# Kernel optimization log

Hardware: AMD Instinct MI355X
Metric: run time of the kernel (lower is better)

## Reference

```python
import jax, jax.numpy as jnp
import numpy as np

B, S, A, C = 32, 52, 3, 80  # batch, grid, anchors-per-cell, classes
EPS_LOG = 1e-16
EPS_IOU = 1e-6
L_CLASS, L_NOOBJ, L_OBJ, L_BOX = 1.0, 10.0, 1.0, 10.0


def setup_inputs() -> dict:
    key = jax.random.key(0)
    k_obj, k_xy, k_wh, k_cls, k_pred, k_anc = jax.random.split(key, 6)
    # target (B,S,S,3,6): [obj_flag, x, y, w, h, class_id]
    obj = (jax.random.uniform(k_obj, (B, S, S, A)) < 0.05).astype(jnp.float32)
    xy = jax.random.uniform(k_xy, (B, S, S, A, 2))
    wh = jax.random.uniform(k_wh, (B, S, S, A, 2), minval=0.1, maxval=2.0)
    cls = jax.random.randint(k_cls, (B, S, S, A), 0, C).astype(jnp.float32)
    target = jnp.concatenate([obj[..., None], xy, wh, cls[..., None]], axis=-1)
    pred = jax.random.normal(k_pred, (B, S, S, A * (C + 5)), dtype=jnp.float32)
    anchors = jax.random.uniform(k_anc, (A, 2), minval=0.5, maxval=2.0)
    return {"target": target, "pred": pred, "anchors": anchors}


def _iou_midpoint(b1, b2):
    # boxes [..., 4] = (cx, cy, w, h)
    b1x1, b1y1 = b1[..., 0] - b1[..., 2] / 2, b1[..., 1] - b1[..., 3] / 2
    b1x2, b1y2 = b1[..., 0] + b1[..., 2] / 2, b1[..., 1] + b1[..., 3] / 2
    b2x1, b2y1 = b2[..., 0] - b2[..., 2] / 2, b2[..., 1] - b2[..., 3] / 2
    b2x2, b2y2 = b2[..., 0] + b2[..., 2] / 2, b2[..., 1] + b2[..., 3] / 2
    iw = jnp.clip(jnp.minimum(b1x2, b2x2) - jnp.maximum(b1x1, b2x1), 0.0)
    ih = jnp.clip(jnp.minimum(b1y2, b2y2) - jnp.maximum(b1y1, b2y1), 0.0)
    inter = iw * ih
    a1 = jnp.abs((b1x2 - b1x1) * (b1y2 - b1y1))
    a2 = jnp.abs((b2x2 - b2x1) * (b2y2 - b2y1))
    return inter / (a1 + a2 - inter + EPS_IOU)


def reference(target, pred, anchors):
    b, s1, s2, k = pred.shape
    prediction = pred.reshape(b, s1, s2, A, k // A)  # (B,S,S,3,C+5)
    obj_f = (target[..., 0] == 1.0).astype(pred.dtype)     # (B,S,S,3)
    noobj_f = (target[..., 0] == 0.0).astype(pred.dtype)
    n_obj = jnp.maximum(jnp.sum(obj_f), 1.0)
    n_noobj = jnp.maximum(jnp.sum(noobj_f), 1.0)

    # ---- no-object BCE (from logits), mean over masked elems ----
    logit_o = prediction[..., 0]
    y = target[..., 0]
    bce = jnp.maximum(logit_o, 0.0) - logit_o * y + jnp.log1p(jnp.exp(-jnp.abs(logit_o)))
    noobjloss = jnp.sum(bce * noobj_f) / n_noobj

    # ---- class sparse CE (from logits), mean over obj cells ----
    logp = jax.nn.log_softmax(prediction[..., 5:], axis=-1)
    labels = target[..., 5].astype(jnp.int32)
    ce = -jnp.take_along_axis(logp, labels[..., None], axis=-1)[..., 0]
    classloss = jnp.sum(ce * obj_f) / n_obj

    # ---- box MSE in transformed space ----
    anc = anchors.reshape(1, 1, 1, A, 2)
    pred_xy = jax.nn.sigmoid(prediction[..., 1:3])
    tgt_wh_log = jnp.log(EPS_LOG + target[..., 3:5] / anc)
    tgt_box = jnp.concatenate([target[..., 1:3], tgt_wh_log], axis=-1)   # (B,S,S,3,4)
    pred_box_reg = jnp.concatenate([pred_xy, prediction[..., 3:5]], axis=-1)
    sq = (tgt_box - pred_box_reg) ** 2
    boxloss = jnp.sum(sq * obj_f[..., None]) / (4.0 * n_obj)

    # ---- objectness MSE against IoU (note: original code compares decoded
    # pred box to the LOG-transformed target wh, faithfully reproduced) ----
    box_pred = jnp.concatenate([pred_xy, jnp.exp(prediction[..., 3:5]) * anc], axis=-1)
    iou = _iou_midpoint(box_pred, tgt_box)                  # (B,S,S,3)
    objloss = jnp.sum(((iou * target[..., 0] - logit_o) ** 2) * obj_f) / n_obj

    return (L_NOOBJ * noobjloss + L_CLASS * classloss
            + L_BOX * boxloss + L_OBJ * objloss)
```

## Files before the change

kernel.cpp:

```cpp
#include <hip/hip_runtime.h>
#include <math.h>

#define BB 32
#define SS 52
#define AA 3
#define CC 80

constexpr int N_CELL = BB * SS * SS;
constexpr int N_ANCH = N_CELL * AA;
constexpr int BLOCK  = 256;
constexpr int NBLK   = N_ANCH / BLOCK;

__device__ __forceinline__ float fast_rcp(float x) {
    return __builtin_amdgcn_rcpf(x);
}


__global__ __launch_bounds__(BLOCK) void yolo_main(
    const float* __restrict__ target,
    const float* __restrict__ pred,
    const float* __restrict__ anchors,
    float* __restrict__ ws)
{
    const int tid  = threadIdx.x;
    const int n    = blockIdx.x * BLOCK + tid;
    const int lane = tid & 63;
    const int grp  = lane >> 4;
    const int l16  = lane & 15;

    const int cell = n / 3;
    const int a    = n - cell * 3;
    const float* t = target + (size_t)n * 6;
    const int poff = cell * 255 + a * 85;

    const float2 t01 = *reinterpret_cast<const float2*>(t);
    const float  l   = pred[poff];
    const bool isobj = (t01.x != 0.0f);

    float2 t23, t45;
    float p1, p2, p3, p4, aw, ah;
    if (isobj) {
        t23 = *reinterpret_cast<const float2*>(t + 2);
        t45 = *reinterpret_cast<const float2*>(t + 4);
        p1 = pred[poff + 1];
        p2 = pred[poff + 2];
        p3 = pred[poff + 3];
        p4 = pred[poff + 4];
        aw = anchors[a * 2 + 0];
        ah = anchors[a * 2 + 1];
    }

    float s_obj = 0.f, s_noobj = 0.f, s_bce = 0.f, s_ce = 0.f, s_sq = 0.f, s_objt = 0.f;
    int label_l = 0;

    if (!isobj) {
        s_noobj = 1.0f;
        s_bce   = fmaxf(l, 0.0f) + __logf(1.0f + __expf(-fabsf(l)));
    } else {
        s_obj   = 1.0f;
        label_l = (int)t45.y;

        float px = fast_rcp(1.0f + __expf(-p1));
        float py = fast_rcp(1.0f + __expf(-p2));
        float tx = t01.y, ty = t23.x;
        float tw = __logf(1e-16f + t23.y * fast_rcp(aw));
        float th = __logf(1e-16f + t45.x * fast_rcp(ah));
        float dx = tx - px, dy = ty - py, dw = tw - p3, dh = th - p4;
        s_sq = dx * dx + dy * dy + dw * dw + dh * dh;

        float bw = __expf(p3) * aw;
        float bh = __expf(p4) * ah;
        float b1x1 = px - bw * 0.5f, b1x2 = px + bw * 0.5f;
        float b1y1 = py - bh * 0.5f, b1y2 = py + bh * 0.5f;
        float b2x1 = tx - tw * 0.5f, b2x2 = tx + tw * 0.5f;
        float b2y1 = ty - th * 0.5f, b2y2 = ty + th * 0.5f;
        float iw = fmaxf(fminf(b1x2, b2x2) - fmaxf(b1x1, b2x1), 0.0f);
        float ih = fmaxf(fminf(b1y2, b2y2) - fmaxf(b1y1, b2y1), 0.0f);
        float inter = iw * ih;
        float a1 = fabsf((b1x2 - b1x1) * (b1y2 - b1y1));
        float a2 = fabsf((b2x2 - b2x1) * (b2y2 - b2y1));
        float iou = inter * fast_rcp(a1 + a2 - inter + 1e-6f);
        float d = iou - l;
        s_objt = d * d;
    }

    unsigned long long m = __ballot(isobj);
    while (m) {
        int b0 = -1, b1 = -1, b2 = -1, b3 = -1;
        if (m) { b0 = __ffsll(m) - 1; m &= m - 1; }
        if (m) { b1 = __ffsll(m) - 1; m &= m - 1; }
        if (m) { b2 = __ffsll(m) - 1; m &= m - 1; }
        if (m) { b3 = __ffsll(m) - 1; m &= m - 1; }
        int src = (grp == 0) ? b0 : (grp == 1) ? b1 : (grp == 2) ? b2 : b3;
        bool active = (src >= 0);
        int s = active ? src : 0;
        int offu  = __shfl(poff, s, 64) + 5;
        int label = __shfl(label_l, s, 64);
        const float* cl = pred + offu + l16 * 5;

        float v0 = 0.f, v1 = 0.f, v2 = 0.f, v3 = 0.f, v4 = 0.f;
        if (active) { v0 = cl[0]; v1 = cl[1]; v2 = cl[2]; v3 = cl[3]; v4 = cl[4]; }

        float mx = fmaxf(fmaxf(fmaxf(v0, v1), fmaxf(v2, v3)), v4);
        #pragma unroll
        for (int o = 8; o > 0; o >>= 1) mx = fmaxf(mx, __shfl_xor(mx, o, 16));

        float se = __expf(v0 - mx) + __expf(v1 - mx) + __expf(v2 - mx)
                 + __expf(v3 - mx) + __expf(v4 - mx);
        #pragma unroll
        for (int o = 8; o > 0; o >>= 1) se += __shfl_xor(se, o, 16);

        int e = label % 5;
        float cand = (e == 0) ? v0 : (e == 1) ? v1 : (e == 2) ? v2
                   : (e == 3) ? v3 : v4;
        float cll  = __shfl(cand, (grp << 4) + label / 5, 64);

        if (active && l16 == 0) s_ce += (mx + __logf(se)) - cll;
    }

    #pragma unroll
    for (int off = 32; off > 0; off >>= 1) {
        s_obj   += __shfl_down(s_obj,   off, 64);
        s_noobj += __shfl_down(s_noobj, off, 64);
        s_bce   += __shfl_down(s_bce,   off, 64);
        s_ce    += __shfl_down(s_ce,    off, 64);
        s_sq    += __shfl_down(s_sq,    off, 64);
        s_objt  += __shfl_down(s_objt,  off, 64);
    }

    __shared__ float red[4][6];
    int wave = tid >> 6;
    if ((tid & 63) == 0) {
        red[wave][0] = s_obj;  red[wave][1] = s_noobj; red[wave][2] = s_bce;
        red[wave][3] = s_ce;   red[wave][4] = s_sq;    red[wave][5] = s_objt;
    }
    __syncthreads();
    if (tid < 6) {
        float v = red[0][tid] + red[1][tid] + red[2][tid] + red[3][tid];
        ws[(size_t)blockIdx.x * 6 + tid] = v;
    }
}

__global__ __launch_bounds__(256) void yolo_final(const float* __restrict__ ws,
                                                  float* __restrict__ out) {
    float acc[6] = {0.f, 0.f, 0.f, 0.f, 0.f, 0.f};
    for (int b = threadIdx.x; b < NBLK; b += 256) {
        const float* p = ws + (size_t)b * 6;
        float2 p01 = *reinterpret_cast<const float2*>(p);
        float2 p23 = *reinterpret_cast<const float2*>(p + 2);
        float2 p45 = *reinterpret_cast<const float2*>(p + 4);
        acc[0] += p01.x; acc[1] += p01.y; acc[2] += p23.x;
        acc[3] += p23.y; acc[4] += p45.x; acc[5] += p45.y;
    }
    #pragma unroll
    for (int off = 32; off > 0; off >>= 1) {
        #pragma unroll
        for (int k = 0; k < 6; ++k) acc[k] += __shfl_down(acc[k], off, 64);
    }
    __shared__ float red[4][6];
    int wave = threadIdx.x >> 6;
    if ((threadIdx.x & 63) == 0) {
        #pragma unroll
        for (int k = 0; k < 6; ++k) red[wave][k] = acc[k];
    }
    __syncthreads();
    if (threadIdx.x == 0) {
        float t[6];
        #pragma unroll
        for (int k = 0; k < 6; ++k)
            t[k] = red[0][k] + red[1][k] + red[2][k] + red[3][k];
        float n_obj   = fmaxf(t[0], 1.0f);
        float n_noobj = fmaxf(t[1], 1.0f);
        float noobjloss = t[2] / n_noobj;
        float classloss = t[3] / n_obj;
        float boxloss   = t[4] / (4.0f * n_obj);
        float objloss   = t[5] / n_obj;
        out[0] = 10.0f * noobjloss + 1.0f * classloss + 10.0f * boxloss + 1.0f * objloss;
    }
}

extern "C" void kernel_launch(void* const* d_in, const int* in_sizes, int n_in,
                              void* d_out, int out_size, void* d_ws, size_t ws_size,
                              hipStream_t stream) {
    const float* target  = (const float*)d_in[0];
    const float* pred    = (const float*)d_in[1];
    const float* anchors = (const float*)d_in[2];
    float* out = (float*)d_out;
    float* ws  = (float*)d_ws;

    hipLaunchKernelGGL(yolo_main, dim3(NBLK), dim3(BLOCK), 0, stream,
                       target, pred, anchors, ws);

    hipLaunchKernelGGL(yolo_final, dim3(1), dim3(256), 0, stream, ws, out);
}
```

Before: 17.43 us.

## Hoist loads and prefetch first class-logit batch before per-anchor math

```diff
diff --git a/kernel.cpp b/kernel.cpp
--- a/kernel.cpp
+++ b/kernel.cpp
@@ -10,6 +10,7 @@
 constexpr int N_ANCH = N_CELL * AA;
 constexpr int BLOCK  = 256;
 constexpr int NBLK   = N_ANCH / BLOCK;
+constexpr int WSCOL  = 1024;
 
 __device__ __forceinline__ float fast_rcp(float x) {
     return __builtin_amdgcn_rcpf(x);
@@ -34,31 +35,41 @@
     const int poff = cell * 255 + a * 85;
 
     const float2 t01 = *reinterpret_cast<const float2*>(t);
-    const float  l   = pred[poff];
+    const float2 t23 = *reinterpret_cast<const float2*>(t + 2);
+    const float2 t45 = *reinterpret_cast<const float2*>(t + 4);
+    const float  p0  = pred[poff];
+    const float  p1  = pred[poff + 1];
+    const float  p2  = pred[poff + 2];
+    const float  p3  = pred[poff + 3];
+    const float  p4  = pred[poff + 4];
+    const float  aw  = anchors[a * 2 + 0];
+    const float  ah  = anchors[a * 2 + 1];
+
     const bool isobj = (t01.x != 0.0f);
-
-    float2 t23, t45;
-    float p1, p2, p3, p4, aw, ah;
-    if (isobj) {
-        t23 = *reinterpret_cast<const float2*>(t + 2);
-        t45 = *reinterpret_cast<const float2*>(t + 4);
-        p1 = pred[poff + 1];
-        p2 = pred[poff + 2];
-        p3 = pred[poff + 3];
-        p4 = pred[poff + 4];
-        aw = anchors[a * 2 + 0];
-        ah = anchors[a * 2 + 1];
-    }
-
-    float s_obj = 0.f, s_noobj = 0.f, s_bce = 0.f, s_ce = 0.f, s_sq = 0.f, s_objt = 0.f;
-    int label_l = 0;
+    const int  label_l = isobj ? (int)t45.y : 0;
+
+    unsigned long long m = __ballot(isobj);
+    int b0 = -1, b1 = -1, b2 = -1, b3 = -1;
+    unsigned long long m2 = m;
+    if (m2) { b0 = __ffsll(m2) - 1; m2 &= m2 - 1; }
+    if (m2) { b1 = __ffsll(m2) - 1; m2 &= m2 - 1; }
+    if (m2) { b2 = __ffsll(m2) - 1; m2 &= m2 - 1; }
+    if (m2) { b3 = __ffsll(m2) - 1; m2 &= m2 - 1; }
+    int  src0 = (grp == 0) ? b0 : (grp == 1) ? b1 : (grp == 2) ? b2 : b3;
+    bool act0 = (src0 >= 0);
+    int  s0   = act0 ? src0 : 0;
+    int  offu0  = __shfl(poff, s0, 64) + 5;
+    int  label0 = __shfl(label_l, s0, 64);
+    const float* cl0 = pred + offu0 + l16 * 5;
+    float w0 = 0.f, w1 = 0.f, w2 = 0.f, w3 = 0.f, w4 = 0.f;
+    if (act0) { w0 = cl0[0]; w1 = cl0[1]; w2 = cl0[2]; w3 = cl0[3]; w4 = cl0[4]; }
+
+    float s_obj = 0.f, s_bce = 0.f, s_ce = 0.f, s_sq = 0.f, s_objt = 0.f;
 
     if (!isobj) {
-        s_noobj = 1.0f;
-        s_bce   = fmaxf(l, 0.0f) + __logf(1.0f + __expf(-fabsf(l)));
+        s_bce = fmaxf(p0, 0.0f) + __logf(1.0f + __expf(-fabsf(p0)));
     } else {
-        s_obj   = 1.0f;
-        label_l = (int)t45.y;
+        s_obj = 1.0f;
 
         float px = fast_rcp(1.0f + __expf(-p1));
         float py = fast_rcp(1.0f + __expf(-p2));
@@ -80,18 +91,35 @@
         float a1 = fabsf((b1x2 - b1x1) * (b1y2 - b1y1));
         float a2 = fabsf((b2x2 - b2x1) * (b2y2 - b2y1));
         float iou = inter * fast_rcp(a1 + a2 - inter + 1e-6f);
-        float d = iou - l;
+        float d = iou - p0;
         s_objt = d * d;
     }
 
-    unsigned long long m = __ballot(isobj);
-    while (m) {
-        int b0 = -1, b1 = -1, b2 = -1, b3 = -1;
-        if (m) { b0 = __ffsll(m) - 1; m &= m - 1; }
-        if (m) { b1 = __ffsll(m) - 1; m &= m - 1; }
-        if (m) { b2 = __ffsll(m) - 1; m &= m - 1; }
-        if (m) { b3 = __ffsll(m) - 1; m &= m - 1; }
-        int src = (grp == 0) ? b0 : (grp == 1) ? b1 : (grp == 2) ? b2 : b3;
+    if (m) {
+        float mx = fmaxf(fmaxf(fmaxf(w0, w1), fmaxf(w2, w3)), w4);
+        #pragma unroll
+        for (int o = 8; o > 0; o >>= 1) mx = fmaxf(mx, __shfl_xor(mx, o, 16));
+
+        float se = __expf(w0 - mx) + __expf(w1 - mx) + __expf(w2 - mx)
+                 + __expf(w3 - mx) + __expf(w4 - mx);
+        #pragma unroll
+        for (int o = 8; o > 0; o >>= 1) se += __shfl_xor(se, o, 16);
+
+        int e = label0 % 5;
+        float cand = (e == 0) ? w0 : (e == 1) ? w1 : (e == 2) ? w2
+                   : (e == 3) ? w3 : w4;
+        float cll  = __shfl(cand, (grp << 4) + label0 / 5, 64);
+
+        if (act0 && l16 == 0) s_ce += (mx + __logf(se)) - cll;
+    }
+
+    while (m2) {
+        int c0 = -1, c1 = -1, c2 = -1, c3 = -1;
+        if (m2) { c0 = __ffsll(m2) - 1; m2 &= m2 - 1; }
+        if (m2) { c1 = __ffsll(m2) - 1; m2 &= m2 - 1; }
+        if (m2) { c2 = __ffsll(m2) - 1; m2 &= m2 - 1; }
+        if (m2) { c3 = __ffsll(m2) - 1; m2 &= m2 - 1; }
+        int src = (grp == 0) ? c0 : (grp == 1) ? c1 : (grp == 2) ? c2 : c3;
         bool active = (src >= 0);
         int s = active ? src : 0;
         int offu  = __shfl(poff, s, 64) + 5;
@@ -120,61 +148,61 @@
 
     #pragma unroll
     for (int off = 32; off > 0; off >>= 1) {
-        s_obj   += __shfl_down(s_obj,   off, 64);
-        s_noobj += __shfl_down(s_noobj, off, 64);
-        s_bce   += __shfl_down(s_bce,   off, 64);
-        s_ce    += __shfl_down(s_ce,    off, 64);
-        s_sq    += __shfl_down(s_sq,    off, 64);
-        s_objt  += __shfl_down(s_objt,  off, 64);
-    }
-
-    __shared__ float red[4][6];
+        s_obj  += __shfl_down(s_obj,  off, 64);
+        s_bce  += __shfl_down(s_bce,  off, 64);
+        s_sq   += __shfl_down(s_sq,   off, 64);
+        s_objt += __shfl_down(s_objt, off, 64);
+    }
+    s_ce += __shfl_down(s_ce, 32, 64);
+    s_ce += __shfl_down(s_ce, 16, 64);
+
+    __shared__ float red[4][5];
     int wave = tid >> 6;
     if ((tid & 63) == 0) {
-        red[wave][0] = s_obj;  red[wave][1] = s_noobj; red[wave][2] = s_bce;
-        red[wave][3] = s_ce;   red[wave][4] = s_sq;    red[wave][5] = s_objt;
+        red[wave][0] = s_obj; red[wave][1] = s_bce; red[wave][2] = s_ce;
+        red[wave][3] = s_sq;  red[wave][4] = s_objt;
     }
     __syncthreads();
-    if (tid < 6) {
+    if (tid < 5) {
         float v = red[0][tid] + red[1][tid] + red[2][tid] + red[3][tid];
-        ws[(size_t)blockIdx.x * 6 + tid] = v;
+        ws[tid * WSCOL + blockIdx.x] = v;
     }
 }
 
 __global__ __launch_bounds__(256) void yolo_final(const float* __restrict__ ws,
                                                   float* __restrict__ out) {
-    float acc[6] = {0.f, 0.f, 0.f, 0.f, 0.f, 0.f};
-    for (int b = threadIdx.x; b < NBLK; b += 256) {
-        const float* p = ws + (size_t)b * 6;
-        float2 p01 = *reinterpret_cast<const float2*>(p);
-        float2 p23 = *reinterpret_cast<const float2*>(p + 2);
-        float2 p45 = *reinterpret_cast<const float2*>(p + 4);
-        acc[0] += p01.x; acc[1] += p01.y; acc[2] += p23.x;
-        acc[3] += p23.y; acc[4] += p45.x; acc[5] += p45.y;
+    float acc[5] = {0.f, 0.f, 0.f, 0.f, 0.f};
+    #pragma unroll
+    for (int r = 0; r < 4; ++r) {
+        int b = threadIdx.x + r * 256;
+        if (b < NBLK) {
+            #pragma unroll
+            for (int k = 0; k < 5; ++k) acc[k] += ws[k * WSCOL + b];
+        }
     }
     #pragma unroll
     for (int off = 32; off > 0; off >>= 1) {
         #pragma unroll
-        for (int k = 0; k < 6; ++k) acc[k] += __shfl_down(acc[k], off, 64);
-    }
-    __shared__ float red[4][6];
+        for (int k = 0; k < 5; ++k) acc[k] += __shfl_down(acc[k], off, 64);
+    }
+    __shared__ float red[4][5];
     int wave = threadIdx.x >> 6;
     if ((threadIdx.x & 63) == 0) {
         #pragma unroll
-        for (int k = 0; k < 6; ++k) red[wave][k] = acc[k];
+        for (int k = 0; k < 5; ++k) red[wave][k] = acc[k];
     }
     __syncthreads();
     if (threadIdx.x == 0) {
-        float t[6];
-        #pragma unroll
-        for (int k = 0; k < 6; ++k)
+        float t[5];
+        #pragma unroll
+        for (int k = 0; k < 5; ++k)
             t[k] = red[0][k] + red[1][k] + red[2][k] + red[3][k];
         float n_obj   = fmaxf(t[0], 1.0f);
-        float n_noobj = fmaxf(t[1], 1.0f);
-        float noobjloss = t[2] / n_noobj;
-        float classloss = t[3] / n_obj;
-        float boxloss   = t[4] / (4.0f * n_obj);
-        float objloss   = t[5] / n_obj;
+        float n_noobj = fmaxf((float)N_ANCH - t[0], 1.0f);
+        float noobjloss = t[1] / n_noobj;
+        float classloss = t[2] / n_obj;
+        float boxloss   = t[3] / (4.0f * n_obj);
+        float objloss   = t[4] / n_obj;
         out[0] = 10.0f * noobjloss + 1.0f * classloss + 10.0f * boxloss + 1.0f * objloss;
     }
 }
```

After: 17.64 us. Within noise of the previous version (+1.2%).
